# Optimization experiments

Hardware: AMD Instinct MI355X
Metric: run time of the kernel (lower is better)

The kernel has to match this reference:

```python
import jax, jax.numpy as jnp
import numpy as np

T, D, F, E, K = 8192, 1024, 4096, 8, 2


def setup_inputs() -> dict:
    key = jax.random.key(0)
    ks = jax.random.split(key, 8)
    s = 0.02
    return {
        "gate_inputs": jax.random.normal(ks[0], (T, D), jnp.float32),
        "inputs": jax.random.normal(ks[1], (T, D), jnp.float32),
        "Wg": jax.random.normal(ks[2], (D, E), jnp.float32) * s,
        "bg": jnp.zeros((E,), jnp.float32),
        "w1": jax.random.normal(ks[3], (E, D, F), jnp.float32) * s,
        "b1": jnp.zeros((E, F), jnp.float32),
        "w2": jax.random.normal(ks[4], (E, F, D), jnp.float32) * s,
        "b2": jnp.zeros((E, D), jnp.float32),
    }


def reference(gate_inputs, inputs, Wg, bg, w1, b1, w2, b2):
    # gate + top-k routing (torch.topk returns sorted descending, as lax.top_k)
    logits = gate_inputs @ Wg + bg                      # [T, E]
    weights, selected = jax.lax.top_k(logits, K)        # [T, K]
    weights = jax.nn.softmax(weights.astype(jnp.float32), axis=1).astype(inputs.dtype)
    # scatter top-k weights into dense combine matrix [T, E]
    t_idx = jnp.arange(inputs.shape[0])[:, None]
    combine = jnp.zeros(logits.shape, inputs.dtype).at[t_idx, selected].add(weights)

    # loop over experts via scan (E is a small structural dim), accumulate weighted outputs
    def body(acc, params):
        W1, B1, W2, B2, ce = params                     # ce: [T] combine weight for this expert
        h = jax.nn.gelu(inputs @ W1 + B1)               # [T, F]
        y = h @ W2 + B2                                 # [T, D]
        return acc + ce[:, None] * y, None

    out, _ = jax.lax.scan(body, jnp.zeros_like(inputs), (w1, b1, w2, b2, combine.T))
    return out
```

## Files before the change

### kernel.cpp

```cpp
#include <hip/hip_runtime.h>
#include <stdint.h>

#define T_TOK 8192
#define DMODEL 1024
#define FDIM 4096
#define NEXP 8
#define NROWS 16384
#define MAXT 80

#define GATE_BLKS 2048
#define CVT_BLKS  4096
#define TR1_BLKS  8192
#define TR2_BLKS  8192
#define PREP_BLKS (GATE_BLKS + CVT_BLKS + TR1_BLKS + TR2_BLKS)

typedef __bf16 bf16x8 __attribute__((ext_vector_type(8)));
typedef float f32x4 __attribute__((ext_vector_type(4)));
#define AS1 __attribute__((address_space(1)))
#define AS3 __attribute__((address_space(3)))

__device__ __forceinline__ unsigned short f2bf(float f) {
  union { float f; unsigned u; } v; v.f = f;
  unsigned r = v.u + 0x7fffu + ((v.u >> 16) & 1u);
  return (unsigned short)(r >> 16);
}
__device__ __forceinline__ float bflo(unsigned u) {
  union { unsigned u; float f; } v; v.u = u << 16; return v.f;
}
__device__ __forceinline__ float bfhi(unsigned u) {
  union { unsigned u; float f; } v; v.u = u & 0xffff0000u; return v.f;
}

__device__ __forceinline__ void transpose_body(
    const float* __restrict__ in, unsigned short* __restrict__ out,
    int R, int C, int bx, int by, int bz, float (*tb)[65])
{
  size_t ebase = (size_t)bz * (size_t)R * (size_t)C;
  int r0 = by * 64, c0 = bx * 64;
#pragma unroll
  for (int p = 0; p < 4; ++p) {
    int item = p * 256 + threadIdx.x;
    int r = item >> 4, c4 = (item & 15) * 4;
    float4 v = *(const float4*)&in[ebase + (size_t)(r0 + r) * C + (c0 + c4)];
    tb[r][c4+0] = v.x; tb[r][c4+1] = v.y; tb[r][c4+2] = v.z; tb[r][c4+3] = v.w;
  }
  __syncthreads();
#pragma unroll
  for (int p = 0; p < 2; ++p) {
    int item = p * 256 + threadIdx.x;
    int c = item >> 3, r8 = (item & 7) * 8;
    union { unsigned short u[8]; uint4 q; } pk;
#pragma unroll
    for (int k = 0; k < 8; ++k) pk.u[k] = f2bf(tb[r8 + k][c]);
    *(uint4*)(out + ebase + (size_t)(c0 + c) * R + (r0 + r8)) = pk.q;
  }
}

__global__ __launch_bounds__(256) void prep_kernel(
    const float* __restrict__ gx, const float* __restrict__ Wg,
    const float* __restrict__ bg, int* __restrict__ sel,
    float* __restrict__ wts, int* __restrict__ counts,
    const float* __restrict__ inputs, unsigned short* __restrict__ Xb,
    const float* __restrict__ w1, unsigned short* __restrict__ W1T,
    const float* __restrict__ w2, unsigned short* __restrict__ W2T)
{
  __shared__ float tb[64][65];
  int b = blockIdx.x;
  if (b < GATE_BLKS) {
    int t = b * 4 + (threadIdx.x >> 6);
    int lane = threadIdx.x & 63;
    const float* row = gx + (size_t)t * DMODEL;
    float acc[NEXP];
#pragma unroll
    for (int e = 0; e < NEXP; ++e) acc[e] = 0.f;
    for (int d = lane; d < DMODEL; d += 64) {
      float x = row[d];
      const float* wgr = Wg + (size_t)d * NEXP;
#pragma unroll
      for (int e = 0; e < NEXP; ++e) acc[e] += x * wgr[e];
    }
#pragma unroll
    for (int off = 32; off > 0; off >>= 1) {
#pragma unroll
      for (int e = 0; e < NEXP; ++e) acc[e] += __shfl_down(acc[e], off);
    }
    if (lane == 0) {
      float lg[NEXP];
#pragma unroll
      for (int e = 0; e < NEXP; ++e) lg[e] = acc[e] + bg[e];
      int i1 = 0; float v1 = lg[0];
#pragma unroll
      for (int e = 1; e < NEXP; ++e) if (lg[e] > v1) { v1 = lg[e]; i1 = e; }
      int i2 = -1; float v2 = -3.4e38f;
#pragma unroll
      for (int e = 0; e < NEXP; ++e) if (e != i1 && lg[e] > v2) { v2 = lg[e]; i2 = e; }
      float ez = __expf(v2 - v1);
      float s = 1.f / (1.f + ez);
      sel[t*2] = i1; sel[t*2+1] = i2;
      wts[t*2] = s;  wts[t*2+1] = ez * s;
      atomicAdd(&counts[i1], 1);
      atomicAdd(&counts[i2], 1);
    }
  } else if (b < GATE_BLKS + CVT_BLKS) {
    int i = (b - GATE_BLKS) * 256 + threadIdx.x;
    const float4* in4 = (const float4*)inputs;
    float4 v0 = in4[(size_t)i*2], v1 = in4[(size_t)i*2 + 1];
    union { unsigned short u[8]; uint4 q; } r;
    r.u[0]=f2bf(v0.x); r.u[1]=f2bf(v0.y); r.u[2]=f2bf(v0.z); r.u[3]=f2bf(v0.w);
    r.u[4]=f2bf(v1.x); r.u[5]=f2bf(v1.y); r.u[6]=f2bf(v1.z); r.u[7]=f2bf(v1.w);
    ((uint4*)Xb)[i] = r.q;
  } else if (b < GATE_BLKS + CVT_BLKS + TR1_BLKS) {
    int bp = b - (GATE_BLKS + CVT_BLKS);
    transpose_body(w1, W1T, DMODEL, FDIM, bp & 63, (bp >> 6) & 15, bp >> 10, tb);
  } else {
    int bp = b - (GATE_BLKS + CVT_BLKS + TR1_BLKS);
    transpose_body(w2, W2T, FDIM, DMODEL, bp & 15, (bp >> 4) & 63, bp >> 10, tb);
  }
}

__global__ __launch_bounds__(256) void scan_build_kernel(
    const int* __restrict__ counts, int* __restrict__ offsets,
    int* __restrict__ ntiles, int* __restrict__ t_e, int* __restrict__ t_r,
    int* __restrict__ t_rend)
{
  __shared__ int sc[8], soff[9], stile[9];
  int tid = threadIdx.x;
  if (tid < 8) sc[tid] = counts[tid];
  __syncthreads();
  if (tid == 0) {
    int off = 0, tl = 0;
#pragma unroll
    for (int e = 0; e < NEXP; ++e) {
      soff[e] = off; stile[e] = tl;
      off += sc[e];
      tl += (sc[e] + 255) >> 8;
    }
    soff[8] = off; stile[8] = tl;
  }
  __syncthreads();
  int ntot = stile[8];
  for (int idx = tid; idx < ntot; idx += 256) {
    int e = 0;
#pragma unroll
    for (int q = 0; q < NEXP; ++q) if (idx >= stile[q + 1]) e = q + 1;
    int r = (idx - stile[e]) * 256;
    t_e[idx] = e; t_r[idx] = soff[e] + r; t_rend[idx] = soff[e] + sc[e];
  }
  if (tid < 9) offsets[tid] = soff[tid];
  if (tid == 0) *ntiles = ntot;
}

__global__ __launch_bounds__(256) void scatter_kernel(
    const int* __restrict__ sel, int* __restrict__ cursors,
    const int* __restrict__ offsets, int* __restrict__ token_list,
    int* __restrict__ slot_list)
{
  int t = blockIdx.x * 256 + threadIdx.x;
  int lane = threadIdx.x & 63;
  unsigned long long ltmask = (lane == 63) ? 0x7fffffffffffffffull
                                           : ((1ull << lane) - 1ull);
#pragma unroll
  for (int k = 0; k < 2; ++k) {
    int e = sel[t*2 + k];
#pragma unroll
    for (int ex = 0; ex < NEXP; ++ex) {
      unsigned long long m = __ballot(e == ex);
      if (m == 0ull) continue;
      if (e == ex) {
        int leader = __ffsll((unsigned long long)m) - 1;
        int cnt = __popcll(m);
        int base = 0;
        if (lane == leader) base = atomicAdd(&cursors[ex], cnt);
        base = __shfl(base, leader);
        int r = offsets[ex] + base + __popcll(m & ltmask);
        token_list[r] = t;
        slot_list[r] = t*2 + k;
      }
    }
  }
}

template<bool G1>
__global__ __launch_bounds__(512, 2) void gemm256_kernel(
    const unsigned short* __restrict__ A, const unsigned short* __restrict__ B,
    const float* __restrict__ b1, const int* __restrict__ token_list,
    const int* __restrict__ slot_list,
    const int* __restrict__ tile_e, const int* __restrict__ tile_r,
    const int* __restrict__ tile_rend, const int* __restrict__ ntiles,
    unsigned short* __restrict__ outp)
{
  constexpr int KDIM = G1 ? DMODEL : FDIM;
  constexpr int NKT  = KDIM / 64;
  constexpr int NOUT = G1 ? FDIM : DMODEL;

  int bid = blockIdx.x;
  int nb, bt;
  if constexpr (G1) {
    int xcd = bid & 7, idx = bid >> 3;
    nb = xcd * 2 + (idx & 1);
    bt = idx >> 1;
  } else {
    nb = bid & 3;
    bt = bid >> 2;
  }
  if (bt >= *ntiles) return;
  const int e = tile_e[bt], row0 = tile_r[bt], rend = tile_rend[bt];
  const int n0 = nb * 256;

  const int tid = threadIdx.x, lane = tid & 63, wave = tid >> 6;
  extern __shared__ __align__(16) char smem[];

  const int lr8 = lane >> 3, g8 = lane & 7, ch = g8 ^ lr8;

  int mA[2], mB[2];
#pragma unroll
  for (int p = 0; p < 2; ++p)
    mA[p] = (wave < 4) ? (p*64 + wave*16) : (128 + p*64 + (wave-4)*16);
#pragma unroll
  for (int nh = 0; nh < 2; ++nh)
    mB[nh] = (wave >> 1)*64 + nh*32 + (wave & 1)*16;

  unsigned aoffs[2][2], boffs[2][2];
#pragma unroll
  for (int p = 0; p < 2; ++p)
#pragma unroll
    for (int l = 0; l < 2; ++l) {
      int m = mA[p] + l*8 + lr8;
      int row = row0 + m; if (row > NROWS - 1) row = NROWS - 1;
      int arow = G1 ? token_list[row] : row;
      aoffs[p][l] = (unsigned)arow * KDIM + ch*8;
      int mb = mB[p] + l*8 + lr8;
      boffs[p][l] = (unsigned)(e * NOUT + n0 + mb) * KDIM + ch*8;
    }

  auto stage_half = [&](int p, int ktn, int bsel) {
    const int kb = ktn * 64;
    char* base = smem + bsel * 65536;
    if (p < 2) {
#pragma unroll
      for (int l = 0; l < 2; ++l)
        __builtin_amdgcn_global_load_lds(
            (const AS1 void*)(A + aoffs[p][l] + kb),
            (AS3 void*)(base + ((mA[p] + l*8) << 7)), 16, 0, 0);
    } else {
      const int nh = p - 2;
#pragma unroll
      for (int l = 0; l < 2; ++l)
        __builtin_amdgcn_global_load_lds(
            (const AS1 void*)(B + boffs[nh][l] + kb),
            (AS3 void*)(base + 32768 + ((mB[nh] + l*8) << 7)), 16, 0, 0);
    }
  };

  f32x4 acc[8][4] = {};
  bf16x8 aR[4][2];
  bf16x8 bR[2][2][2];
  const int wr = wave >> 2, wc = wave & 3;
  const int lm = lane & 15, lk = lane >> 4, l7 = lane & 7;
  const unsigned abase = (unsigned)(wr*128 + lm) * 128;
  const unsigned bbase = 32768u + (unsigned)(wc*64 + lm) * 128;
  const unsigned kx0 = (unsigned)((lk ^ l7) << 4);
  const unsigned kx1 = (unsigned)(((4 + lk) ^ l7) << 4);

  auto rdA = [&](const char* base, int mh) {
#pragma unroll
    for (int i = 0; i < 4; ++i) {
      const char* pA = base + abase + mh*8192 + i*2048;
      aR[i][0] = *(const bf16x8*)(pA + kx0);
      aR[i][1] = *(const bf16x8*)(pA + kx1);
    }
  };
  auto rdB = [&](const char* base, int nh) {
#pragma unroll
    for (int jj = 0; jj < 2; ++jj) {
      const char* pB = base + bbase + nh*4096 + jj*2048;
      bR[nh][jj][0] = *(const bf16x8*)(pB + kx0);
      bR[nh][jj][1] = *(const bf16x8*)(pB + kx1);
    }
  };
  auto mm = [&](int mh, int nh) {
    __builtin_amdgcn_s_setprio(1);
#pragma unroll
    for (int i = 0; i < 4; ++i)
#pragma unroll
      for (int jj = 0; jj < 2; ++jj) {
        acc[mh*4+i][nh*2+jj] = __builtin_amdgcn_mfma_f32_16x16x32_bf16(
            aR[i][0], bR[nh][jj][0], acc[mh*4+i][nh*2+jj], 0, 0, 0);
        acc[mh*4+i][nh*2+jj] = __builtin_amdgcn_mfma_f32_16x16x32_bf16(
            aR[i][1], bR[nh][jj][1], acc[mh*4+i][nh*2+jj], 0, 0, 0);
      }
    __builtin_amdgcn_s_setprio(0);
  };

  stage_half(0, 0, 0);
  stage_half(2, 0, 0);
  stage_half(3, 0, 0);
  stage_half(1, 0, 0);

  for (int kt = 0; kt < NKT; ++kt) {
    const int b = kt & 1;
    const int nxt = b ^ 1;
    const char* base = smem + b * 65536;
    const bool pre = (kt + 1 < NKT);
    if (pre) {
      stage_half(0, kt + 1, nxt);
      asm volatile("s_waitcnt vmcnt(6)" ::: "memory");
    } else {
      asm volatile("s_waitcnt vmcnt(4)" ::: "memory");
    }
    __builtin_amdgcn_s_barrier();
    __builtin_amdgcn_sched_barrier(0);
    rdA(base, 0); rdB(base, 0);
    asm volatile("s_waitcnt lgkmcnt(0)" ::: "memory");
    __builtin_amdgcn_sched_barrier(0);
    mm(0, 0);
    __builtin_amdgcn_s_barrier();
    if (pre) {
      stage_half(2, kt + 1, nxt);
      asm volatile("s_waitcnt vmcnt(6)" ::: "memory");
    } else {
      asm volatile("s_waitcnt vmcnt(2)" ::: "memory");
    }
    __builtin_amdgcn_s_barrier();
    __builtin_amdgcn_sched_barrier(0);
    rdB(base, 1);
    asm volatile("s_waitcnt lgkmcnt(0)" ::: "memory");
    __builtin_amdgcn_sched_barrier(0);
    mm(0, 1);
    __builtin_amdgcn_s_barrier();
    if (pre) {
      stage_half(3, kt + 1, nxt);
      asm volatile("s_waitcnt vmcnt(6)" ::: "memory");
    } else {
      asm volatile("s_waitcnt vmcnt(0)" ::: "memory");
    }
    __builtin_amdgcn_s_barrier();
    __builtin_amdgcn_sched_barrier(0);
    rdA(base, 1);
    asm volatile("s_waitcnt lgkmcnt(0)" ::: "memory");
    __builtin_amdgcn_sched_barrier(0);
    mm(1, 1);
    __builtin_amdgcn_s_barrier();
    if (pre) stage_half(1, kt + 1, nxt);
    mm(1, 0);
    __builtin_amdgcn_s_barrier();
    __builtin_amdgcn_sched_barrier(0);
  }

  asm volatile("" ::: "memory");
  float bias[4] = {};
  if constexpr (G1) {
#pragma unroll
    for (int j = 0; j < 4; ++j) bias[j] = b1[(size_t)e * FDIM + n0 + wc*64 + j*16 + lm];
  }

  float* eps = (float*)smem;
#pragma unroll
  for (int c = 0; c < 8; ++c) {
    __syncthreads();
    if (wr == (c >> 2)) {
#pragma unroll
      for (int ii = 0; ii < 2; ++ii) {
        const int mi = (c & 3) * 2 + ii;
#pragma unroll
        for (int j = 0; j < 4; ++j) {
#pragma unroll
          for (int r = 0; r < 4; ++r) {
            float v = acc[mi][j][r];
            if constexpr (G1) {
              v += bias[j];
              float z2 = 1.5957691216f * (v + 0.044715f * v * v * v);
              v = v / (1.f + __expf(-z2));
            }
            eps[(ii*16 + lk*4 + r) * 260 + wc*64 + j*16 + lm] = v;
          }
        }
      }
    }
    __syncthreads();
#pragma unroll
    for (int u = 0; u < 2; ++u) {
      int item = u * 512 + tid;
      int lrow = item >> 5, c8 = (item & 31) * 8;
      int gr = row0 + c * 32 + lrow;
      if (gr < rend) {
        float4 v0 = *(const float4*)&eps[lrow * 260 + c8];
        float4 v1 = *(const float4*)&eps[lrow * 260 + c8 + 4];
        union { unsigned short u[8]; uint4 q; } pk;
        pk.u[0]=f2bf(v0.x); pk.u[1]=f2bf(v0.y); pk.u[2]=f2bf(v0.z); pk.u[3]=f2bf(v0.w);
        pk.u[4]=f2bf(v1.x); pk.u[5]=f2bf(v1.y); pk.u[6]=f2bf(v1.z); pk.u[7]=f2bf(v1.w);
        size_t orow;
        if constexpr (G1) orow = (size_t)gr * FDIM;
        else              orow = (size_t)slot_list[gr] * DMODEL;
        *(uint4*)(outp + orow + n0 + c8) = pk.q;
      }
    }
  }
}

__global__ __launch_bounds__(256) void combine_kernel(
    const unsigned short* __restrict__ ys, const float* __restrict__ wts,
    const int* __restrict__ sel, const float* __restrict__ b2,
    float* __restrict__ out)
{
  int i = blockIdx.x * 256 + threadIdx.x;
  int t = i >> 7, d8 = i & 127;
  float w0 = wts[t*2], w1 = wts[t*2 + 1];
  int e0 = sel[t*2], e1 = sel[t*2 + 1];
  const uint4* ys4 = (const uint4*)ys;
  uint4 ya = ys4[(size_t)(t*2) * 128 + d8];
  uint4 yb = ys4[(size_t)(t*2 + 1) * 128 + d8];
  const float4* b24 = (const float4*)b2;
  float4 c0a = b24[e0*256 + d8*2], c0b = b24[e0*256 + d8*2 + 1];
  float4 c1a = b24[e1*256 + d8*2], c1b = b24[e1*256 + d8*2 + 1];
  float4 o0, o1;
  o0.x = w0*(bflo(ya.x)+c0a.x) + w1*(bflo(yb.x)+c1a.x);
  o0.y = w0*(bfhi(ya.x)+c0a.y) + w1*(bfhi(yb.x)+c1a.y);
  o0.z = w0*(bflo(ya.y)+c0a.z) + w1*(bflo(yb.y)+c1a.z);
  o0.w = w0*(bfhi(ya.y)+c0a.w) + w1*(bfhi(yb.y)+c1a.w);
  o1.x = w0*(bflo(ya.z)+c0b.x) + w1*(bflo(yb.z)+c1b.x);
  o1.y = w0*(bfhi(ya.z)+c0b.y) + w1*(bfhi(yb.z)+c1b.y);
  o1.z = w0*(bflo(ya.w)+c0b.z) + w1*(bflo(yb.w)+c1b.z);
  o1.w = w0*(bfhi(ya.w)+c0b.w) + w1*(bfhi(yb.w)+c1b.w);
  float4* out4 = (float4*)out;
  out4[(size_t)t * 256 + d8*2]     = o0;
  out4[(size_t)t * 256 + d8*2 + 1] = o1;
}

extern "C" void kernel_launch(void* const* d_in, const int* in_sizes, int n_in,
                              void* d_out, int out_size, void* d_ws, size_t ws_size,
                              hipStream_t stream)
{
  const float* gate_inputs = (const float*)d_in[0];
  const float* inputs      = (const float*)d_in[1];
  const float* Wg          = (const float*)d_in[2];
  const float* bg          = (const float*)d_in[3];
  const float* w1          = (const float*)d_in[4];
  const float* b1          = (const float*)d_in[5];
  const float* w2          = (const float*)d_in[6];
  const float* b2          = (const float*)d_in[7];
  float* out = (float*)d_out;

  char* ws = (char*)d_ws;
  size_t o = 0;
  auto carve = [&](size_t bytes) { void* p = ws + o; o += (bytes + 255) & ~(size_t)255; return p; };
  unsigned short* Xb  = (unsigned short*)carve((size_t)T_TOK * DMODEL * 2);
  unsigned short* W1T = (unsigned short*)carve((size_t)NEXP * FDIM * DMODEL * 2);
  unsigned short* W2T = (unsigned short*)carve((size_t)NEXP * DMODEL * FDIM * 2);
  unsigned short* H   = (unsigned short*)carve((size_t)NROWS * FDIM * 2);
  unsigned short* ys  = (unsigned short*)carve((size_t)NROWS * DMODEL * 2);
  int*   sel          = (int*)carve((size_t)NROWS * 4);
  float* wts          = (float*)carve((size_t)NROWS * 4);
  int*   token_list   = (int*)carve((size_t)(NROWS + 256) * 4);
  int*   slot_list    = (int*)carve((size_t)(NROWS + 256) * 4);
  int*   ctrl         = (int*)carve(4096);
  int* counts  = ctrl;
  int* cursors = ctrl + 8;
  int* offsets = ctrl + 16;
  int* ntiles  = ctrl + 28;
  int* t_e     = ctrl + 32;
  int* t_r     = ctrl + 32 + MAXT;
  int* t_rend  = ctrl + 32 + 2 * MAXT;

  hipMemsetAsync(counts, 0, 64, stream);

  prep_kernel<<<PREP_BLKS, 256, 0, stream>>>(
      gate_inputs, Wg, bg, sel, wts, counts,
      inputs, Xb, w1, W1T, w2, W2T);
  scan_build_kernel<<<1, 256, 0, stream>>>(counts, offsets, ntiles, t_e, t_r, t_rend);
  scatter_kernel<<<T_TOK / 256, 256, 0, stream>>>(sel, cursors, offsets, token_list, slot_list);

  hipFuncSetAttribute((const void*)gemm256_kernel<true>,
                      hipFuncAttributeMaxDynamicSharedMemorySize, 131072);
  hipFuncSetAttribute((const void*)gemm256_kernel<false>,
                      hipFuncAttributeMaxDynamicSharedMemorySize, 131072);
  gemm256_kernel<true><<<8 * 2 * MAXT, 512, 131072, stream>>>(
      Xb, W1T, b1, token_list, nullptr, t_e, t_r, t_rend, ntiles, H);
  gemm256_kernel<false><<<4 * MAXT, 512, 131072, stream>>>(
      H, W2T, nullptr, nullptr, slot_list, t_e, t_r, t_rend, ntiles, ys);
  combine_kernel<<<(T_TOK * DMODEL / 8) / 256, 256, 0, stream>>>(ys, wts, sel, b2, out);
}
```

Measured before the change: 706.0 us.

## Store transposed expert weights in K-chunked layout for contiguous B tile loads

```diff
diff --git a/kernel.cpp b/kernel.cpp
--- a/kernel.cpp
+++ b/kernel.cpp
@@ -10,8 +10,8 @@
 
 #define GATE_BLKS 2048
 #define CVT_BLKS  4096
-#define TR1_BLKS  8192
-#define TR2_BLKS  8192
+#define TR1_BLKS  4096
+#define TR2_BLKS  4096
 #define PREP_BLKS (GATE_BLKS + CVT_BLKS + TR1_BLKS + TR2_BLKS)
 
 typedef __bf16 bf16x8 __attribute__((ext_vector_type(8)));
@@ -31,28 +31,28 @@
   union { unsigned u; float f; } v; v.u = u & 0xffff0000u; return v.f;
 }
 
-__device__ __forceinline__ void transpose_body(
+__device__ __forceinline__ void transpose_chunk_body(
     const float* __restrict__ in, unsigned short* __restrict__ out,
-    int R, int C, int bx, int by, int bz, float (*tb)[65])
-{
-  size_t ebase = (size_t)bz * (size_t)R * (size_t)C;
-  int r0 = by * 64, c0 = bx * 64;
-#pragma unroll
-  for (int p = 0; p < 4; ++p) {
+    int Kdim, int Ndim, int bx, int by, int bz, float (*tb)[133])
+{
+  size_t ebase = (size_t)bz * (size_t)Kdim * (size_t)Ndim;
+  int k0 = by * 64, n0 = bx * 128;
+#pragma unroll
+  for (int p = 0; p < 8; ++p) {
     int item = p * 256 + threadIdx.x;
-    int r = item >> 4, c4 = (item & 15) * 4;
-    float4 v = *(const float4*)&in[ebase + (size_t)(r0 + r) * C + (c0 + c4)];
+    int r = item >> 5, c4 = (item & 31) * 4;
+    float4 v = *(const float4*)&in[ebase + (size_t)(k0 + r) * Ndim + n0 + c4];
     tb[r][c4+0] = v.x; tb[r][c4+1] = v.y; tb[r][c4+2] = v.z; tb[r][c4+3] = v.w;
   }
   __syncthreads();
 #pragma unroll
-  for (int p = 0; p < 2; ++p) {
-    int item = p * 256 + threadIdx.x;
-    int c = item >> 3, r8 = (item & 7) * 8;
-    union { unsigned short u[8]; uint4 q; } pk;
-#pragma unroll
-    for (int k = 0; k < 8; ++k) pk.u[k] = f2bf(tb[r8 + k][c]);
-    *(uint4*)(out + ebase + (size_t)(c0 + c) * R + (r0 + r8)) = pk.q;
+  for (int q = 0; q < 4; ++q) {
+    int item = q * 256 + threadIdx.x;
+    int n = item >> 3, k8 = (item & 7) * 8;
+    union { unsigned short u[8]; uint4 v4; } pk;
+#pragma unroll
+    for (int j = 0; j < 8; ++j) pk.u[j] = f2bf(tb[k8 + j][n]);
+    *(uint4*)(out + ebase + ((size_t)by * Ndim + n0 + n) * 64 + k8) = pk.v4;
   }
 }
 
@@ -64,7 +64,7 @@
     const float* __restrict__ w1, unsigned short* __restrict__ W1T,
     const float* __restrict__ w2, unsigned short* __restrict__ W2T)
 {
-  __shared__ float tb[64][65];
+  __shared__ float tb[64][133];
   int b = blockIdx.x;
   if (b < GATE_BLKS) {
     int t = b * 4 + (threadIdx.x >> 6);
@@ -111,10 +111,10 @@
     ((uint4*)Xb)[i] = r.q;
   } else if (b < GATE_BLKS + CVT_BLKS + TR1_BLKS) {
     int bp = b - (GATE_BLKS + CVT_BLKS);
-    transpose_body(w1, W1T, DMODEL, FDIM, bp & 63, (bp >> 6) & 15, bp >> 10, tb);
+    transpose_chunk_body(w1, W1T, DMODEL, FDIM, bp & 31, (bp >> 5) & 15, bp >> 9, tb);
   } else {
     int bp = b - (GATE_BLKS + CVT_BLKS + TR1_BLKS);
-    transpose_body(w2, W2T, FDIM, DMODEL, bp & 15, (bp >> 4) & 63, bp >> 10, tb);
+    transpose_chunk_body(w2, W2T, FDIM, DMODEL, bp & 7, (bp >> 3) & 63, bp >> 9, tb);
   }
 }
 
@@ -192,6 +192,7 @@
   constexpr int KDIM = G1 ? DMODEL : FDIM;
   constexpr int NKT  = KDIM / 64;
   constexpr int NOUT = G1 ? FDIM : DMODEL;
+  constexpr int KTB  = NOUT * 64;
 
   int bid = blockIdx.x;
   int nb, bt;
@@ -220,6 +221,7 @@
   for (int nh = 0; nh < 2; ++nh)
     mB[nh] = (wave >> 1)*64 + nh*32 + (wave & 1)*16;
 
+  const unsigned short* eB = B + (size_t)e * KDIM * NOUT;
   unsigned aoffs[2][2], boffs[2][2];
 #pragma unroll
   for (int p = 0; p < 2; ++p)
@@ -230,13 +232,13 @@
       int arow = G1 ? token_list[row] : row;
       aoffs[p][l] = (unsigned)arow * KDIM + ch*8;
       int mb = mB[p] + l*8 + lr8;
-      boffs[p][l] = (unsigned)(e * NOUT + n0 + mb) * KDIM + ch*8;
+      boffs[p][l] = (unsigned)((n0 + mb) * 64 + ch*8);
     }
 
   auto stage_half = [&](int p, int ktn, int bsel) {
-    const int kb = ktn * 64;
     char* base = smem + bsel * 65536;
     if (p < 2) {
+      const int kb = ktn * 64;
 #pragma unroll
       for (int l = 0; l < 2; ++l)
         __builtin_amdgcn_global_load_lds(
@@ -244,10 +246,11 @@
             (AS3 void*)(base + ((mA[p] + l*8) << 7)), 16, 0, 0);
     } else {
       const int nh = p - 2;
+      const unsigned short* bk = eB + (size_t)ktn * KTB;
 #pragma unroll
       for (int l = 0; l < 2; ++l)
         __builtin_amdgcn_global_load_lds(
-            (const AS1 void*)(B + boffs[nh][l] + kb),
+            (const AS1 void*)(bk + boffs[nh][l]),
             (AS3 void*)(base + 32768 + ((mB[nh] + l*8) << 7)), 16, 0, 0);
     }
   };
```

New measurement: 698.9 us. No clear change (-1.0%).
